# Kernel tuning notes

Measured on AMD Instinct MI355X. Metric: run time of the kernel, lower is better.

## Reference

```python
import jax, jax.numpy as jnp
import numpy as np

HEADS = 30
HEAD_DIM = 64
DIM = HEADS * HEAD_DIM  # 1920
TXT = 226
VID = 2048
EPS = 1e-5


def setup_inputs() -> dict:
    key = jax.random.key(0)
    ks = jax.random.split(key, 12)
    s = 1.0 / np.sqrt(DIM)
    return {
        "hidden_states": jax.random.normal(ks[0], (1, VID, DIM), jnp.float32),
        "encoder_hidden_states": jax.random.normal(ks[1], (1, TXT, DIM), jnp.float32),
        "rope_cos": jax.random.uniform(ks[2], (VID, HEAD_DIM), jnp.float32, -1.0, 1.0),
        "rope_sin": jax.random.uniform(ks[3], (VID, HEAD_DIM), jnp.float32, -1.0, 1.0),
        "Wq": jax.random.normal(ks[4], (DIM, DIM), jnp.float32) * s,
        "bq": jnp.zeros((DIM,), jnp.float32),
        "Wk": jax.random.normal(ks[5], (DIM, DIM), jnp.float32) * s,
        "bk": jnp.zeros((DIM,), jnp.float32),
        "Wv": jax.random.normal(ks[6], (DIM, DIM), jnp.float32) * s,
        "bv": jnp.zeros((DIM,), jnp.float32),
        "ln_q_w": jnp.ones((HEAD_DIM,), jnp.float32),
        "ln_q_b": jnp.zeros((HEAD_DIM,), jnp.float32),
        "ln_k_w": jnp.ones((HEAD_DIM,), jnp.float32),
        "ln_k_b": jnp.zeros((HEAD_DIM,), jnp.float32),
        "Wo": jax.random.normal(ks[7], (DIM, DIM), jnp.float32) * s,
        "bo": jnp.zeros((DIM,), jnp.float32),
    }


def _layernorm(x, w, b):
    mu = jnp.mean(x, axis=-1, keepdims=True)
    var = jnp.var(x, axis=-1, keepdims=True)
    return (x - mu) * jax.lax.rsqrt(var + EPS) * w + b


def _apply_rope(x, cos, sin):
    # x: [B,H,S_vid,D]; cos/sin: [S_vid,D]. Interleaved-pair rotation (diffusers use_real, unbind_dim=-1).
    xr = x[..., 0::2]
    xi = x[..., 1::2]
    rot = jnp.stack([-xi, xr], axis=-1).reshape(x.shape)
    return x * cos + rot * sin


def reference(hidden_states, encoder_hidden_states, rope_cos, rope_sin,
              Wq, bq, Wk, bk, Wv, bv, ln_q_w, ln_q_b, ln_k_w, ln_k_b, Wo, bo):
    T = encoder_hidden_states.shape[1]
    h = jnp.concatenate([encoder_hidden_states, hidden_states], axis=1)  # [B,S,D]
    B, S, _ = h.shape

    def proj(W, bias):
        y = h @ W.T + bias
        return y.reshape(B, S, HEADS, HEAD_DIM).transpose(0, 2, 1, 3)  # [B,H,S,d]

    q = proj(Wq, bq)
    k = proj(Wk, bk)
    v = proj(Wv, bv)

    q = _layernorm(q, ln_q_w, ln_q_b)
    k = _layernorm(k, ln_k_w, ln_k_b)

    # rotary embedding applied only to the image/video tokens
    q = jnp.concatenate([q[:, :, :T], _apply_rope(q[:, :, T:], rope_cos, rope_sin)], axis=2)
    k = jnp.concatenate([k[:, :, :T], _apply_rope(k[:, :, T:], rope_cos, rope_sin)], axis=2)

    scale = 1.0 / np.sqrt(HEAD_DIM)
    scores = jnp.einsum("bhqd,bhkd->bhqk", q, k) * scale
    attn = jax.nn.softmax(scores, axis=-1)
    out = jnp.einsum("bhqk,bhkd->bhqd", attn, v)

    out = out.transpose(0, 2, 1, 3).reshape(B, S, DIM)
    out = out @ Wo.T + bo
    return out[:, T:], out[:, :T]
```

## Files before the change

### kernel.cpp

```cpp
#include <hip/hip_runtime.h>
#include <hip/hip_bf16.h>

typedef __hip_bfloat16 bf16;
using f32x4 = __attribute__((ext_vector_type(4))) float;
using f32x16 = __attribute__((ext_vector_type(16))) float;
using s16x8 = __attribute__((ext_vector_type(8))) short;

#define S_TOT 2274
#define S_PAD 2304
#define TTXT 226
#define DIMN 1920
#define NH 30
#define HD 64
#define NQKV 5760
#define QSCALE 0.1803368801f
#define NSPLIT 3
#define SMAX 20.0f

#define GLOAD_LDS16(g, l)                                                              \
  __builtin_amdgcn_global_load_lds((const __attribute__((address_space(1))) void*)(g), \
                                   (__attribute__((address_space(3))) void*)(l), 16, 0, 0)

__global__ void k_prep_all(const float* __restrict__ hid, const float* __restrict__ enc,
                           const float* __restrict__ Wq, const float* __restrict__ Wk,
                           const float* __restrict__ Wv, const float* __restrict__ Wo,
                           bf16* __restrict__ h_bf, bf16* __restrict__ wqkv,
                           bf16* __restrict__ wo_bf) {
  const long T1 = (long)S_PAD * DIMN;
  const long PER = (long)DIMN * DIMN;
  long i4 = ((long)blockIdx.x * blockDim.x + threadIdx.x) * 4;
  if (i4 >= T1 + 4 * PER) return;
  float4 v = make_float4(0.f, 0.f, 0.f, 0.f);
  bf16* dst;
  long di;
  if (i4 < T1) {
    int s = (int)(i4 / DIMN);
    if (s < TTXT)
      v = *reinterpret_cast<const float4*>(enc + i4);
    else if (s < S_TOT)
      v = *reinterpret_cast<const float4*>(hid + i4 - (long)TTXT * DIMN);
    dst = h_bf;
    di = i4;
  } else if (i4 < T1 + 3 * PER) {
    const long j = i4 - T1;
    const float* src = (j < PER) ? (Wq + j) : (j < 2 * PER) ? (Wk + j - PER) : (Wv + j - 2 * PER);
    v = *reinterpret_cast<const float4*>(src);
    dst = wqkv;
    di = j;
  } else {
    const long j = i4 - T1 - 3 * PER;
    v = *reinterpret_cast<const float4*>(Wo + j);
    dst = wo_bf;
    di = j;
  }
  union {
    bf16 b[4];
    short4 s4;
  } o;
  o.b[0] = __float2bfloat16(v.x);
  o.b[1] = __float2bfloat16(v.y);
  o.b[2] = __float2bfloat16(v.z);
  o.b[3] = __float2bfloat16(v.w);
  *reinterpret_cast<short4*>(dst + di) = o.s4;
}

#define NKT32 60
#define QBUF 24576
__global__ __launch_bounds__(512, 4) void k_gemm_qkv9(
    const bf16* __restrict__ A, const bf16* __restrict__ B, const float* __restrict__ bq,
    const float* __restrict__ bk, const float* __restrict__ bv, const float* __restrict__ lqw,
    const float* __restrict__ lqb, const float* __restrict__ lkw, const float* __restrict__ lkb,
    const float* __restrict__ cosT, const float* __restrict__ sinT, bf16* __restrict__ qb,
    bf16* __restrict__ kbf, bf16* __restrict__ vt) {
  __shared__ __align__(16) char smem[3 * QBUF];
  const int tid = threadIdx.x;
  const int w = tid >> 6, lane = tid & 63;
  const int clo = lane & 15, lhi = lane >> 4;
  const int wr = w >> 1, wc = w & 1;
  const int m0 = blockIdx.y * 256, n0 = blockIdx.x * 128;

  const int u1 = 512 + tid;
  const long ga0 = (long)(m0 + (tid >> 2)) * DIMN + (((tid & 3) ^ ((tid >> 2) & 3)) * 8);
  const long ga1 = (long)(m0 + (u1 >> 2)) * DIMN + (((u1 & 3) ^ ((u1 >> 2) & 3)) * 8);
  const long gb0 = (long)(n0 + (tid >> 2)) * DIMN + (((tid & 3) ^ ((tid >> 2) & 3)) * 8);
  const int wbase = w * 1024;

  auto stage = [&](int b, int kt) {
    char* Ab = &smem[b * QBUF];
    char* Bb = Ab + 16384;
    const int ko = kt * 32;
    GLOAD_LDS16(A + ga0 + ko, Ab + wbase);
    GLOAD_LDS16(A + ga1 + ko, Ab + 8192 + wbase);
    GLOAD_LDS16(B + gb0 + ko, Bb + wbase);
  };

  auto rdf = [&](const char* base, int row) {
    return *reinterpret_cast<const s16x8*>(base + row * 64 + ((lhi ^ (row & 3)) * 16));
  };

  f32x4 acc[4][4] = {};

  stage(0, 0);
  stage(1, 1);
  for (int t = 0; t < NKT32; ++t) {
    if (t < NKT32 - 1)
      asm volatile("s_waitcnt vmcnt(3)" ::: "memory");
    else
      asm volatile("s_waitcnt vmcnt(0)" ::: "memory");
    __builtin_amdgcn_s_barrier();
    if (t + 2 < NKT32) stage((t + 2) % 3, t + 2);
    const char* Ab = &smem[(t % 3) * QBUF];
    const char* Bb = Ab + 16384;
    s16x8 af[4], bfr[4];
#pragma unroll
    for (int m = 0; m < 4; ++m) af[m] = rdf(Ab, wr * 64 + m * 16 + clo);
#pragma unroll
    for (int n = 0; n < 4; ++n) bfr[n] = rdf(Bb, wc * 64 + n * 16 + clo);
    __builtin_amdgcn_s_setprio(1);
#pragma unroll
    for (int m = 0; m < 4; ++m)
#pragma unroll
      for (int n = 0; n < 4; ++n)
        acc[m][n] = __builtin_amdgcn_mfma_f32_16x16x32_bf16(af[m], bfr[n], acc[m][n], 0, 0, 0);
    __builtin_amdgcn_s_setprio(0);
  }
  __syncthreads();

  const int gcol0 = n0 + wc * 64;
  const int sect = gcol0 / DIMN;
  const int hcol = gcol0 - sect * DIMN;
  const int head = hcol >> 6;
  const int row0 = m0 + wr * 64;

  if (sect < 2) {
    const float* bias = sect ? bk : bq;
    const float* lw = sect ? lkw : lqw;
    const float* lb = sect ? lkb : lqb;
    bf16* dst = sect ? kbf : qb;
    const float oscale = sect ? 1.f : QSCALE;
    float bb[4], lww[4], lbb[4];
#pragma unroll
    for (int n = 0; n < 4; ++n) {
      const int d = (n << 4) + clo;
      bb[n] = bias[hcol + d];
      lww[n] = lw[d];
      lbb[n] = lb[d];
    }
#pragma unroll
    for (int m = 0; m < 4; ++m) {
#pragma unroll
      for (int r = 0; r < 4; ++r) {
        const int row = row0 + m * 16 + lhi * 4 + r;
        float x[4];
#pragma unroll
        for (int n = 0; n < 4; ++n) x[n] = acc[m][n][r] + bb[n];
        float s_ = (x[0] + x[1]) + (x[2] + x[3]);
        float q_ = x[0] * x[0];
        q_ = fmaf(x[1], x[1], q_);
        q_ = fmaf(x[2], x[2], q_);
        q_ = fmaf(x[3], x[3], q_);
#pragma unroll
        for (int off = 1; off <= 8; off <<= 1) {
          s_ += __shfl_xor(s_, off);
          q_ += __shfl_xor(q_, off);
        }
        const float mu = s_ * (1.f / 64.f);
        const float var = q_ * (1.f / 64.f) - mu * mu;
        const float rst = rsqrtf(var + 1e-5f);
        float xn[4];
#pragma unroll
        for (int n = 0; n < 4; ++n) xn[n] = (x[n] - mu) * rst * lww[n] + lbb[n];
        const bool dorope = (row >= TTXT) && (row < S_TOT);
        if (dorope) {
          const float* cr = cosT + (long)(row - TTXT) * HD;
          const float* sr2 = sinT + (long)(row - TTXT) * HD;
#pragma unroll
          for (int n = 0; n < 4; ++n) {
            const int d = (n << 4) + clo;
            const float p = __shfl_xor(xn[n], 1);
            xn[n] = xn[n] * cr[d] + ((clo & 1) ? p : -p) * sr2[d];
          }
        }
#pragma unroll
        for (int n = 0; n < 4; ++n)
          dst[((long)head * S_PAD + row) * HD + (n << 4) + clo] =
              __float2bfloat16(xn[n] * oscale);
      }
    }
  } else {
    float bb[4];
#pragma unroll
    for (int n = 0; n < 4; ++n) bb[n] = bv[hcol + (n << 4) + clo];
    bf16* Lp = reinterpret_cast<bf16*>(smem + w * 9216);
#pragma unroll
    for (int m = 0; m < 4; ++m)
#pragma unroll
      for (int n = 0; n < 4; ++n)
#pragma unroll
        for (int r = 0; r < 4; ++r)
          Lp[((n << 4) + clo) * 72 + m * 16 + lhi * 4 + r] =
              __float2bfloat16(acc[m][n][r] + bb[n]);
    const int dsub = lane >> 3, sc = lane & 7;
#pragma unroll
    for (int it = 0; it < 8; ++it) {
      const int d = it * 8 + dsub;
      s16x8 v = *reinterpret_cast<const s16x8*>(&Lp[d * 72 + sc * 8]);
      *reinterpret_cast<s16x8*>(vt + ((long)head * HD + d) * S_PAD + row0 + sc * 8) = v;
    }
  }
}

__global__ __launch_bounds__(256, 4) void k_gemm_proj9(const bf16* __restrict__ A,
                                                       const bf16* __restrict__ B,
                                                       float* __restrict__ C,
                                                       const float* __restrict__ bias) {
  __shared__ __align__(16) char smem[3 * 12288];
  const int tid = threadIdx.x;
  const int w = tid >> 6, lane = tid & 63;
  const int clo = lane & 15, lhi = lane >> 4;
  const int wr = w >> 1, wc = w & 1;
  const int m0 = blockIdx.y * 128, n0 = blockIdx.x * 64;

  const int u1 = 256 + tid;
  const long ga0 = (long)(m0 + (tid >> 2)) * DIMN + (((tid & 3) ^ ((tid >> 2) & 3)) * 8);
  const long ga1 = (long)(m0 + (u1 >> 2)) * DIMN + (((u1 & 3) ^ ((u1 >> 2) & 3)) * 8);
  const long gb0 = (long)(n0 + (tid >> 2)) * DIMN + (((tid & 3) ^ ((tid >> 2) & 3)) * 8);
  const int wbase = w * 1024;

  auto stage = [&](int b, int kt) {
    char* Ab = &smem[b * 12288];
    char* Bb = Ab + 8192;
    const int ko = kt * 32;
    GLOAD_LDS16(A + ga0 + ko, Ab + wbase);
    GLOAD_LDS16(A + ga1 + ko, Ab + 4096 + wbase);
    GLOAD_LDS16(B + gb0 + ko, Bb + wbase);
  };

  auto rdf = [&](const char* base, int row) {
    return *reinterpret_cast<const s16x8*>(base + row * 64 + ((lhi ^ (row & 3)) * 16));
  };

  f32x4 acc[4][2] = {};

  stage(0, 0);
  stage(1, 1);
  for (int t = 0; t < NKT32; ++t) {
    if (t < NKT32 - 1)
      asm volatile("s_waitcnt vmcnt(3)" ::: "memory");
    else
      asm volatile("s_waitcnt vmcnt(0)" ::: "memory");
    __builtin_amdgcn_s_barrier();
    if (t + 2 < NKT32) stage((t + 2) % 3, t + 2);
    const char* Ab = &smem[(t % 3) * 12288];
    const char* Bb = Ab + 8192;
    s16x8 af[4], bfr[2];
#pragma unroll
    for (int m = 0; m < 4; ++m) af[m] = rdf(Ab, wr * 64 + m * 16 + clo);
#pragma unroll
    for (int n = 0; n < 2; ++n) bfr[n] = rdf(Bb, wc * 32 + n * 16 + clo);
    __builtin_amdgcn_s_setprio(1);
#pragma unroll
    for (int m = 0; m < 4; ++m)
#pragma unroll
      for (int n = 0; n < 2; ++n)
        acc[m][n] = __builtin_amdgcn_mfma_f32_16x16x32_bf16(af[m], bfr[n], acc[m][n], 0, 0, 0);
    __builtin_amdgcn_s_setprio(0);
  }
#pragma unroll
  for (int n = 0; n < 2; ++n) {
    const int col = n0 + wc * 32 + n * 16 + clo;
    const float bvv = bias[col];
#pragma unroll
    for (int m = 0; m < 4; ++m) {
#pragma unroll
      for (int r = 0; r < 4; ++r) {
        const int row = m0 + wr * 64 + m * 16 + lhi * 4 + r;
        if (row < S_TOT) {
          const int dst = (row >= TTXT) ? (row - TTXT) : (row + (S_TOT - TTXT));
          C[(long)dst * DIMN + col] = acc[m][n][r] + bvv;
        }
      }
    }
  }
}

__global__ __launch_bounds__(512, 4) void k_flash11(const bf16* __restrict__ qb,
                                                    const bf16* __restrict__ kbf,
                                                    const bf16* __restrict__ vt,
                                                    float* __restrict__ po,
                                                    float* __restrict__ pl) {
  __shared__ __align__(16) char smem[32768];
  const int h = blockIdx.x, qt = blockIdx.y, ks = blockIdx.z;
  const int tid = threadIdx.x, w = tid >> 6, lane = tid & 63;
  const int l31 = lane & 31, hf = lane >> 5;
  const bf16* Qh = qb + (long)h * S_PAD * HD;
  const bf16* Kh = kbf + (long)h * S_PAD * HD;
  const bf16* Vh = vt + (long)h * HD * S_PAD;
  const int q0w = qt * 256 + w * 32;
  const int T0 = ks * 12;

  s16x8 qf[4];
#pragma unroll
  for (int t = 0; t < 4; ++t)
    qf[t] = *reinterpret_cast<const s16x8*>(Qh + (long)(q0w + l31) * HD + t * 16 + hf * 8);

  f32x16 accO[2] = {};
  f32x16 lacc = {};

  const s16x8 ones8 = {0x3F80, 0x3F80, 0x3F80, 0x3F80, 0x3F80, 0x3F80, 0x3F80, 0x3F80};

  const int sr = tid >> 3, sc8 = tid & 7;
  const long kg0 = (long)sr * HD + ((sc8 ^ (sr & 7)) * 8);
  const long vg0 = (long)sr * S_PAD + ((sc8 ^ (sr & 7)) * 8);
  const int ldsb = w * 1024;

  auto stage = [&](int b, int kb0) {
    char* Kb = &smem[b * 16384];
    char* Vb = &smem[b * 16384 + 8192];
    GLOAD_LDS16(Kh + (long)kb0 * HD + kg0, Kb + ldsb);
    GLOAD_LDS16(Vh + kb0 + vg0, Vb + ldsb);
  };

  auto ldsrd = [&](const char* base, int row, int c) {
    return *reinterpret_cast<const s16x8*>(base + row * 128 + ((c ^ (row & 7)) * 16));
  };
  auto pk2 = [&](float a, float b) -> unsigned {
    __hip_bfloat162 t = __float22bfloat162_rn(make_float2(a, b));
    return *reinterpret_cast<unsigned*>(&t);
  };

  stage(0, T0 * 64);
  __syncthreads();
  int cur = 0;
  for (int kt = 0; kt < 12; ++kt) {
    const int kb0 = (T0 + kt) * 64;
    if (kt + 1 < 12) stage(cur ^ 1, kb0 + 64);
    const char* Kb = &smem[cur * 16384];
    const char* Vb = &smem[cur * 16384 + 8192];

    f32x16 s0 = {}, s1 = {};
#pragma unroll
    for (int t = 0; t < 4; ++t) {
      s16x8 k0 = ldsrd(Kb, l31, 2 * t + hf);
      s16x8 k1 = ldsrd(Kb, 32 + l31, 2 * t + hf);
      s0 = __builtin_amdgcn_mfma_f32_32x32x16_bf16(k0, qf[t], s0, 0, 0, 0);
      s1 = __builtin_amdgcn_mfma_f32_32x32x16_bf16(k1, qf[t], s1, 0, 0, 0);
    }
    if (kb0 + 64 > S_TOT) {
#pragma unroll
      for (int j = 0; j < 16; ++j) {
        const int key = kb0 + (j & 3) + 8 * (j >> 2) + 4 * hf;
        if (key >= S_TOT) s0[j] = -1e30f;
        if (key + 32 >= S_TOT) s1[j] = -1e30f;
      }
    }
#pragma unroll
    for (int j = 0; j < 16; ++j) {
      s0[j] = exp2f(s0[j] - SMAX);
      s1[j] = exp2f(s1[j] - SMAX);
    }
    unsigned gw0[8], gw1[8];
#pragma unroll
    for (int i = 0; i < 4; ++i) {
      gw0[2 * i] = pk2(s0[4 * i], s0[4 * i + 1]);
      gw0[2 * i + 1] = pk2(s0[4 * i + 2], s0[4 * i + 3]);
      gw1[2 * i] = pk2(s1[4 * i], s1[4 * i + 1]);
      gw1[2 * i + 1] = pk2(s1[4 * i + 2], s1[4 * i + 3]);
    }
    s16x8 pa[4];
#pragma unroll
    for (int b = 0; b < 2; ++b) {
      unsigned* gw = b ? gw1 : gw0;
#pragma unroll
      for (int t = 0; t < 2; ++t) {
        auto rA = __builtin_amdgcn_permlane32_swap(gw[4 * t + 0], gw[4 * t + 2], false, false);
        auto rB = __builtin_amdgcn_permlane32_swap(gw[4 * t + 1], gw[4 * t + 3], false, false);
        union {
          unsigned u[4];
          s16x8 v;
        } A;
        A.u[0] = rA[0];
        A.u[1] = rB[0];
        A.u[2] = rA[1];
        A.u[3] = rB[1];
        pa[b * 2 + t] = A.v;
      }
    }
#pragma unroll
    for (int t4 = 0; t4 < 4; ++t4) {
      s16x8 v0 = ldsrd(Vb, l31, 2 * t4 + hf);
      s16x8 v1 = ldsrd(Vb, 32 + l31, 2 * t4 + hf);
      accO[0] = __builtin_amdgcn_mfma_f32_32x32x16_bf16(pa[t4], v0, accO[0], 0, 0, 0);
      accO[1] = __builtin_amdgcn_mfma_f32_32x32x16_bf16(pa[t4], v1, accO[1], 0, 0, 0);
      lacc = __builtin_amdgcn_mfma_f32_32x32x16_bf16(pa[t4], ones8, lacc, 0, 0, 0);
    }
    __syncthreads();
    cur ^= 1;
  }
  const long rowbase = ((long)(ks * NH + h)) * S_PAD + q0w;
  if (l31 == 0) {
#pragma unroll
    for (int j = 0; j < 16; ++j) pl[rowbase + (j & 3) + 8 * (j >> 2) + 4 * hf] = lacc[j];
  }
#pragma unroll
  for (int j = 0; j < 16; ++j) {
    const int pat = (j & 3) + 8 * (j >> 2) + 4 * hf;
    float* dst = po + (rowbase + pat) * HD + l31;
    dst[0] = accO[0][j];
    dst[32] = accO[1][j];
  }
}

__global__ __launch_bounds__(256) void k_combine3(const float* __restrict__ po,
                                                  const float* __restrict__ pl,
                                                  bf16* __restrict__ ao) {
  const int idx = blockIdx.x * 256 + threadIdx.x;
  const int d4 = (idx & 15) * 4;
  const int row = (idx >> 4) % S_PAD;
  const int h = idx / (S_PAD * 16);
  if (row >= S_TOT) return;
  float4 o = make_float4(0.f, 0.f, 0.f, 0.f);
  float l = 0.f;
#pragma unroll
  for (int i = 0; i < NSPLIT; ++i) {
    const long r = ((long)(i * NH + h)) * S_PAD + row;
    const float4 p = *reinterpret_cast<const float4*>(po + r * HD + d4);
    o.x += p.x;
    o.y += p.y;
    o.z += p.z;
    o.w += p.w;
    l += pl[r];
  }
  const float inv = 1.f / l;
  union {
    bf16 b[4];
    short4 s4;
  } ob;
  ob.b[0] = __float2bfloat16(o.x * inv);
  ob.b[1] = __float2bfloat16(o.y * inv);
  ob.b[2] = __float2bfloat16(o.z * inv);
  ob.b[3] = __float2bfloat16(o.w * inv);
  *reinterpret_cast<short4*>(ao + (long)row * DIMN + h * HD + d4) = ob.s4;
}

extern "C" void kernel_launch(void* const* d_in, const int* in_sizes, int n_in, void* d_out,
                              int out_size, void* d_ws, size_t ws_size, hipStream_t stream) {
  const float* hid = (const float*)d_in[0];
  const float* enc = (const float*)d_in[1];
  const float* rc = (const float*)d_in[2];
  const float* rs = (const float*)d_in[3];
  const float* Wq = (const float*)d_in[4];
  const float* bq = (const float*)d_in[5];
  const float* Wk = (const float*)d_in[6];
  const float* bk = (const float*)d_in[7];
  const float* Wv = (const float*)d_in[8];
  const float* bv = (const float*)d_in[9];
  const float* lqw = (const float*)d_in[10];
  const float* lqb = (const float*)d_in[11];
  const float* lkw = (const float*)d_in[12];
  const float* lkb = (const float*)d_in[13];
  const float* Wo = (const float*)d_in[14];
  const float* bo = (const float*)d_in[15];
  float* out = (float*)d_out;

  char* ws = (char*)d_ws;
  size_t off = 0;
  float* po = (float*)(ws + off);
  off += (size_t)NSPLIT * NH * S_PAD * HD * 4;
  bf16* h_bf = (bf16*)(ws + off);
  off += (size_t)S_PAD * DIMN * 2;
  bf16* wqkv = (bf16*)(ws + off);
  off += (size_t)3 * DIMN * DIMN * 2;
  bf16* wo = (bf16*)(ws + off);
  off += (size_t)DIMN * DIMN * 2;
  bf16* q_bf = (bf16*)(ws + off);
  off += (size_t)NH * S_PAD * HD * 2;
  bf16* k_bf = (bf16*)(ws + off);
  off += (size_t)NH * S_PAD * HD * 2;
  bf16* vt_bf = (bf16*)(ws + off);
  off += (size_t)NH * HD * S_PAD * 2;
  bf16* at_bf = (bf16*)(ws + off);
  off += (size_t)S_PAD * DIMN * 2;

  float* pl = (float*)h_bf;

  const long PREP_N = ((long)S_PAD * DIMN + 4L * DIMN * DIMN) / 4;
  k_prep_all<<<(int)((PREP_N + 255) / 256), 256, 0, stream>>>(hid, enc, Wq, Wk, Wv, Wo, h_bf,
                                                              wqkv, wo);
  k_gemm_qkv9<<<dim3(NQKV / 128, S_PAD / 256), 512, 0, stream>>>(
      h_bf, wqkv, bq, bk, bv, lqw, lqb, lkw, lkb, rc, rs, q_bf, k_bf, vt_bf);
  k_flash11<<<dim3(NH, S_PAD / 256, NSPLIT), 512, 0, stream>>>(q_bf, k_bf, vt_bf, po, pl);
  k_combine3<<<NH * S_PAD * 16 / 256, 256, 0, stream>>>(po, pl, at_bf);
  k_gemm_proj9<<<dim3(DIMN / 64, S_PAD / 128), 256, 0, stream>>>(at_bf, wo, out, bo);
}
```

Baseline: 221.0 us.

## Swizzle GEMM tiles across XCDs and replace MFMA row-sum with VALU reduction

Both GEMM kernels remap workgroup IDs so that consecutive tiles sharing A/B panels land on the same XCD, aiming to improve L2 reuse on the multi-die MI355X. The flash kernel drops the extra MFMA with a ones-vector that computed softmax row sums. Instead it sums the exponentiated scores in registers and combines the two half-waves with a permlane32 swap. This removes one matrix op per k-step and replaces it with VALU adds. It also assumes the lane layout of s0/s1 maps each row's values to a single lane plus its swap partner.

Result: no change. 222.6 us (+0.7%).

```diff
diff --git a/kernel.cpp b/kernel.cpp
--- a/kernel.cpp
+++ b/kernel.cpp
@@ -20,6 +20,12 @@
 #define GLOAD_LDS16(g, l)                                                              \
   __builtin_amdgcn_global_load_lds((const __attribute__((address_space(1))) void*)(g), \
                                    (__attribute__((address_space(3))) void*)(l), 16, 0, 0)
+
+__device__ __forceinline__ int xcd_swz(int orig, int nwg) {
+  const int q = nwg >> 3, r = nwg & 7;
+  const int xcd = orig & 7, pos = orig >> 3;
+  return (xcd < r ? xcd * (q + 1) : r * (q + 1) + (xcd - r) * q) + pos;
+}
 
 __global__ void k_prep_all(const float* __restrict__ hid, const float* __restrict__ enc,
                            const float* __restrict__ Wq, const float* __restrict__ Wk,
@@ -66,7 +72,7 @@
 
 #define NKT32 60
 #define QBUF 24576
-__global__ __launch_bounds__(512, 4) void k_gemm_qkv9(
+__global__ __launch_bounds__(512, 4) void k_gemm_qkv10(
     const bf16* __restrict__ A, const bf16* __restrict__ B, const float* __restrict__ bq,
     const float* __restrict__ bk, const float* __restrict__ bv, const float* __restrict__ lqw,
     const float* __restrict__ lqb, const float* __restrict__ lkw, const float* __restrict__ lkb,
@@ -77,7 +83,8 @@
   const int w = tid >> 6, lane = tid & 63;
   const int clo = lane & 15, lhi = lane >> 4;
   const int wr = w >> 1, wc = w & 1;
-  const int m0 = blockIdx.y * 256, n0 = blockIdx.x * 128;
+  const int swz = xcd_swz(blockIdx.y * 45 + blockIdx.x, 405);
+  const int m0 = (swz / 45) * 256, n0 = (swz % 45) * 128;
 
   const int u1 = 512 + tid;
   const long ga0 = (long)(m0 + (tid >> 2)) * DIMN + (((tid & 3) ^ ((tid >> 2) & 3)) * 8);
@@ -210,16 +217,17 @@
   }
 }
 
-__global__ __launch_bounds__(256, 4) void k_gemm_proj9(const bf16* __restrict__ A,
-                                                       const bf16* __restrict__ B,
-                                                       float* __restrict__ C,
-                                                       const float* __restrict__ bias) {
+__global__ __launch_bounds__(256, 4) void k_gemm_proj10(const bf16* __restrict__ A,
+                                                        const bf16* __restrict__ B,
+                                                        float* __restrict__ C,
+                                                        const float* __restrict__ bias) {
   __shared__ __align__(16) char smem[3 * 12288];
   const int tid = threadIdx.x;
   const int w = tid >> 6, lane = tid & 63;
   const int clo = lane & 15, lhi = lane >> 4;
   const int wr = w >> 1, wc = w & 1;
-  const int m0 = blockIdx.y * 128, n0 = blockIdx.x * 64;
+  const int swz = xcd_swz(blockIdx.y * 30 + blockIdx.x, 540);
+  const int m0 = (swz / 30) * 128, n0 = (swz % 30) * 64;
 
   const int u1 = 256 + tid;
   const long ga0 = (long)(m0 + (tid >> 2)) * DIMN + (((tid & 3) ^ ((tid >> 2) & 3)) * 8);
@@ -284,7 +292,7 @@
   }
 }
 
-__global__ __launch_bounds__(512, 4) void k_flash11(const bf16* __restrict__ qb,
+__global__ __launch_bounds__(512, 4) void k_flash13(const bf16* __restrict__ qb,
                                                     const bf16* __restrict__ kbf,
                                                     const bf16* __restrict__ vt,
                                                     float* __restrict__ po,
@@ -305,9 +313,7 @@
     qf[t] = *reinterpret_cast<const s16x8*>(Qh + (long)(q0w + l31) * HD + t * 16 + hf * 8);
 
   f32x16 accO[2] = {};
-  f32x16 lacc = {};
-
-  const s16x8 ones8 = {0x3F80, 0x3F80, 0x3F80, 0x3F80, 0x3F80, 0x3F80, 0x3F80, 0x3F80};
+  float l_run = 0.f;
 
   const int sr = tid >> 3, sc8 = tid & 7;
   const long kg0 = (long)sr * HD + ((sc8 ^ (sr & 7)) * 8);
@@ -358,6 +364,18 @@
     for (int j = 0; j < 16; ++j) {
       s0[j] = exp2f(s0[j] - SMAX);
       s1[j] = exp2f(s1[j] - SMAX);
+    }
+    {
+      float ts[16];
+#pragma unroll
+      for (int j = 0; j < 16; ++j) ts[j] = s0[j] + s1[j];
+#pragma unroll
+      for (int st = 8; st >= 1; st >>= 1)
+#pragma unroll
+        for (int i = 0; i < st; ++i) ts[i] += ts[i + st];
+      auto r = __builtin_amdgcn_permlane32_swap(__float_as_uint(ts[0]), __float_as_uint(ts[0]),
+                                                false, false);
+      l_run += __uint_as_float(r[0]) + __uint_as_float(r[1]);
     }
     unsigned gw0[8], gw1[8];
 #pragma unroll
@@ -392,16 +410,12 @@
       s16x8 v1 = ldsrd(Vb, 32 + l31, 2 * t4 + hf);
       accO[0] = __builtin_amdgcn_mfma_f32_32x32x16_bf16(pa[t4], v0, accO[0], 0, 0, 0);
       accO[1] = __builtin_amdgcn_mfma_f32_32x32x16_bf16(pa[t4], v1, accO[1], 0, 0, 0);
-      lacc = __builtin_amdgcn_mfma_f32_32x32x16_bf16(pa[t4], ones8, lacc, 0, 0, 0);
     }
     __syncthreads();
     cur ^= 1;
   }
   const long rowbase = ((long)(ks * NH + h)) * S_PAD + q0w;
-  if (l31 == 0) {
-#pragma unroll
-    for (int j = 0; j < 16; ++j) pl[rowbase + (j & 3) + 8 * (j >> 2) + 4 * hf] = lacc[j];
-  }
+  if (hf == 0) pl[rowbase + l31] = l_run;
 #pragma unroll
   for (int j = 0; j < 16; ++j) {
     const int pat = (j & 3) + 8 * (j >> 2) + 4 * hf;
@@ -487,9 +501,9 @@
   const long PREP_N = ((long)S_PAD * DIMN + 4L * DIMN * DIMN) / 4;
   k_prep_all<<<(int)((PREP_N + 255) / 256), 256, 0, stream>>>(hid, enc, Wq, Wk, Wv, Wo, h_bf,
                                                               wqkv, wo);
-  k_gemm_qkv9<<<dim3(NQKV / 128, S_PAD / 256), 512, 0, stream>>>(
-      h_bf, wqkv, bq, bk, bv, lqw, lqb, lkw, lkb, rc, rs, q_bf, k_bf, vt_bf);
-  k_flash11<<<dim3(NH, S_PAD / 256, NSPLIT), 512, 0, stream>>>(q_bf, k_bf, vt_bf, po, pl);
+  k_gemm_qkv10<<<dim3(45, 9), 512, 0, stream>>>(h_bf, wqkv, bq, bk, bv, lqw, lqb, lkw, lkb, rc,
+                                                rs, q_bf, k_bf, vt_bf);
+  k_flash13<<<dim3(NH, S_PAD / 256, NSPLIT), 512, 0, stream>>>(q_bf, k_bf, vt_bf, po, pl);
   k_combine3<<<NH * S_PAD * 16 / 256, 256, 0, stream>>>(po, pl, at_bf);
-  k_gemm_proj9<<<dim3(DIMN / 64, S_PAD / 128), 256, 0, stream>>>(at_bf, wo, out, bo);
-}
+  k_gemm_proj10<<<dim3(30, 18), 256, 0, stream>>>(at_bf, wo, out, bo);
+}
```
